# Optimization experiments

Measured on AMD Instinct MI355X. Metric: run time of the kernel, lower is better.

Reference implementation:

```python
import jax, jax.numpy as jnp
import numpy as np

NEG = -1.0e9

def setup_inputs() -> dict:
    key = jax.random.key(0)
    ks = jax.random.split(key, 4)
    B, S, D, DK = 4, 2048, 1024, 128
    inputs = jax.random.normal(ks[0], (B, S, D), dtype=jnp.float32)
    scale = 1.0 / np.sqrt(D)
    Wq = jax.random.normal(ks[1], (D, DK), dtype=jnp.float32) * scale
    Wk = jax.random.normal(ks[2], (D, DK), dtype=jnp.float32) * scale
    Wv = jax.random.normal(ks[3], (D, DK), dtype=jnp.float32) * scale
    bq = jnp.zeros((DK,), dtype=jnp.float32)
    bk = jnp.zeros((DK,), dtype=jnp.float32)
    bv = jnp.zeros((DK,), dtype=jnp.float32)
    return {"inputs": inputs, "Wq": Wq, "bq": bq, "Wk": Wk, "bk": bk, "Wv": Wv, "bv": bv}

def reference(inputs, Wq, bq, Wk, bk, Wv, bv):
    # Q/K/V projections: Dense(d_k) on last dim
    Q = jnp.einsum('bsd,dk->bsk', inputs, Wq) + bq
    K = jnp.einsum('bsd,dk->bsk', inputs, Wk) + bk
    V = jnp.einsum('bsd,dk->bsk', inputs, Wv) + bv
    d_k = Q.shape[-1]
    S = inputs.shape[1]
    # FAITHFUL to original bug: mask = lower-triangular ones, added *-1e9
    # (masks the lower triangle including the diagonal, NOT the upper).
    mask = jnp.tril(jnp.ones((S, S), dtype=inputs.dtype))
    scores = jnp.einsum('bqk,bsk->bqs', Q, K) / jnp.sqrt(jnp.asarray(d_k, inputs.dtype))
    masked_scores = scores + mask * NEG  # [B, S, S]
    attn = jax.nn.softmax(masked_scores, axis=-1)
    out = jnp.einsum('bqs,bsk->bqk', attn, V)  # [B, S, d_k]
    return out
```

## Files before the change

### kernel.cpp

```cpp
#include <hip/hip_runtime.h>
#include <hip/hip_bf16.h>

typedef __attribute__((ext_vector_type(8))) short bf16x8;
typedef __attribute__((ext_vector_type(4))) float f32x4;

#define QSCALE 0.088388347648318447f

__device__ __forceinline__ unsigned short f2bf(float f) {
  __hip_bfloat16 h = __float2bfloat16(f);
  unsigned short u;
  __builtin_memcpy(&u, &h, 2);
  return u;
}
__device__ __forceinline__ float bf2f(unsigned short u) {
  unsigned int x = ((unsigned int)u) << 16;
  float f; __builtin_memcpy(&f, &x, 4);
  return f;
}

__device__ __forceinline__ void gload_lds16(void* lds, const void* g) {
  __builtin_amdgcn_global_load_lds(
      (const __attribute__((address_space(1))) unsigned int*)g,
      (__attribute__((address_space(3))) unsigned int*)lds, 16, 0, 0);
}

__global__ __launch_bounds__(256) void cvt(const float* __restrict__ x,
                                           unsigned short* __restrict__ xb,
                                           const float* __restrict__ Wq,
                                           const float* __restrict__ Wk,
                                           const float* __restrict__ Wv,
                                           unsigned short* __restrict__ Wt) {
  const int bid = blockIdx.x;
  if (bid < 4096) {
    int i = (bid * 256 + threadIdx.x) * 8;
    float4 v0 = *reinterpret_cast<const float4*>(x + i);
    float4 v1 = *reinterpret_cast<const float4*>(x + i + 4);
    ushort4 o0, o1;
    o0.x = f2bf(v0.x); o0.y = f2bf(v0.y); o0.z = f2bf(v0.z); o0.w = f2bf(v0.w);
    o1.x = f2bf(v1.x); o1.y = f2bf(v1.y); o1.z = f2bf(v1.z); o1.w = f2bf(v1.w);
    *reinterpret_cast<ushort4*>(xb + i) = o0;
    *reinterpret_cast<ushort4*>(xb + i + 4) = o1;
  } else {
    int idx = (bid - 4096) * 256 + threadIdx.x;
    int n = idx >> 10, d = idx & 1023;
    const float* W = (n < 128) ? Wq : (n < 256 ? Wk : Wv);
    float v = W[d * 128 + (n & 127)];
    if (n < 128) v *= QSCALE;
    Wt[idx] = f2bf(v);
  }
}

__global__ __launch_bounds__(256) void proj_gemm(
    const unsigned short* __restrict__ Xb, const unsigned short* __restrict__ Wt,
    const float* __restrict__ bq, const float* __restrict__ bk, const float* __restrict__ bv,
    unsigned short* __restrict__ Qb, unsigned short* __restrict__ Kb,
    unsigned short* __restrict__ Vt) {
  __shared__ unsigned short sA[64 * 64];
  __shared__ unsigned short sB[64 * 64];
  const int nt = blockIdx.x % 6;
  const int mt = blockIdx.x / 6;
  const int m0 = mt * 64;
  const int n0 = nt * 64;
  const int tid = threadIdx.x;
  const int lane = tid & 63;
  const int w = tid >> 6;
  const int r = lane & 15, g = lane >> 4;
  const int wm = (w >> 1) * 32, wn = (w & 1) * 32;

  f32x4 acc[2][2];
  #pragma unroll
  for (int mi = 0; mi < 2; ++mi)
    #pragma unroll
    for (int ni = 0; ni < 2; ++ni)
      acc[mi][ni] = (f32x4){0.f, 0.f, 0.f, 0.f};

  const char* Ab = (const char*)Xb;
  const char* Bb = (const char*)Wt;
  char* sAb = (char*)sA;
  char* sBb = (char*)sB;

  for (int k0 = 0; k0 < 1024; k0 += 64) {
    #pragma unroll
    for (int j = 0; j < 2; ++j) {
      int f = j * 4096 + tid * 16;
      int row = f >> 7;
      int colb = f & 127;
      gload_lds16(sAb + f, Ab + ((size_t)(m0 + row) * 1024 + k0) * 2 + colb);
      gload_lds16(sBb + f, Bb + ((size_t)(n0 + row) * 1024 + k0) * 2 + colb);
    }
    __syncthreads();
    #pragma unroll
    for (int kk = 0; kk < 2; ++kk) {
      bf16x8 af[2], bfr[2];
      #pragma unroll
      for (int mi = 0; mi < 2; ++mi)
        af[mi] = *reinterpret_cast<const bf16x8*>(sA + (wm + mi * 16 + r) * 64 + kk * 32 + g * 8);
      #pragma unroll
      for (int ni = 0; ni < 2; ++ni)
        bfr[ni] = *reinterpret_cast<const bf16x8*>(sB + (wn + ni * 16 + r) * 64 + kk * 32 + g * 8);
      #pragma unroll
      for (int mi = 0; mi < 2; ++mi)
        #pragma unroll
        for (int ni = 0; ni < 2; ++ni)
          acc[mi][ni] = __builtin_amdgcn_mfma_f32_16x16x32_bf16(af[mi], bfr[ni], acc[mi][ni], 0, 0, 0);
    }
    __syncthreads();
  }

  const float* bias = (nt < 2) ? bq : (nt < 4 ? bk : bv);
  const float bsc = (nt < 2) ? QSCALE : 1.0f;
  #pragma unroll
  for (int mi = 0; mi < 2; ++mi) {
    #pragma unroll
    for (int ni = 0; ni < 2; ++ni) {
      const int colg = n0 + wn + ni * 16 + r;
      const int colm = colg & 127;
      const float bias_v = bias[colm] * bsc;
      #pragma unroll
      for (int e = 0; e < 4; ++e) {
        const int row = m0 + wm + mi * 16 + g * 4 + e;
        const unsigned short hh = f2bf(acc[mi][ni][e] + bias_v);
        if (nt < 2) Qb[(size_t)row * 128 + colm] = hh;
        else if (nt < 4) Kb[(size_t)row * 128 + colm] = hh;
        else {
          const int bb = row >> 11, s = row & 2047;
          Vt[((size_t)bb * 128 + colm) * 2048 + s] = hh;
        }
      }
    }
  }
}

__global__ __launch_bounds__(512, 4) void attn(
    const unsigned short* __restrict__ Qb, const unsigned short* __restrict__ Kb,
    const unsigned short* __restrict__ Vt,
    float* __restrict__ po, float* __restrict__ pl) {
  __shared__ char sK[2][8192];
  __shared__ char sV[2][8192];
  __shared__ unsigned short pbuf_s[8][512];
  const int tid = threadIdx.x;
  const int lane = tid & 63;
  const int w = tid >> 6;
  const int r = lane & 15, g = lane >> 4;
  const int sig = blockIdx.x & 7;
  const int b = (blockIdx.x >> 3) & 3;
  const int p = blockIdx.x >> 5;

  const char* Kg = (const char*)(Kb + (size_t)b * 2048 * 128);
  const char* Vg = (const char*)(Vt + (size_t)b * 128 * 2048);
  unsigned short* pbuf = pbuf_s[w];

  const int krow = tid >> 4;
  const int kcol = ((tid & 15) * 16) ^ ((krow & 7) * 16);
  const int vrow = tid >> 2;
  const int vcol = ((tid & 3) * 16) ^ ((vrow & 3) * 16);

  for (int phase = 0; phase < 2; ++phase) {
    const int t = phase ? (15 - p) : p;
    const int q0b = t << 7;
    const int ntiles = (2048 - q0b) >> 5;
    const int q0w = q0b + w * 16;

    const unsigned short* Q = Qb + (size_t)(b * 2048 + q0w) * 128;
    bf16x8 qf[4];
    #pragma unroll
    for (int kk = 0; kk < 4; ++kk)
      qf[kk] = *reinterpret_cast<const bf16x8*>(Q + r * 128 + kk * 32 + g * 8);

    f32x4 o[8];
    #pragma unroll
    for (int ni = 0; ni < 8; ++ni) o[ni] = (f32x4){0.f, 0.f, 0.f, 0.f};
    float l[4];
    #pragma unroll
    for (int e = 0; e < 4; ++e) l[e] = 0.f;

    const int nT = (ntiles > sig) ? ((ntiles - sig + 7) >> 3) : 0;

    if (nT > 0) {
      const int s0 = q0b + (sig << 5);
      gload_lds16(&sK[0][tid * 16], Kg + (size_t)(s0 + krow) * 256 + kcol);
      gload_lds16(&sV[0][tid * 16], Vg + (size_t)vrow * 4096 + (size_t)s0 * 2 + vcol);
    }
    for (int it = 0; it < nT; ++it) {
      const int cur = it & 1;
      const int s0 = q0b + ((sig + (it << 3)) << 5);
      if (it + 1 < nT) {
        const int s1 = s0 + 256;
        gload_lds16(&sK[cur ^ 1][tid * 16], Kg + (size_t)(s1 + krow) * 256 + kcol);
        gload_lds16(&sV[cur ^ 1][tid * 16], Vg + (size_t)vrow * 4096 + (size_t)s1 * 2 + vcol);
        asm volatile("s_waitcnt vmcnt(2)" ::: "memory");
      } else {
        asm volatile("s_waitcnt vmcnt(0)" ::: "memory");
      }
      asm volatile("s_barrier" ::: "memory");

      f32x4 st[2];
      #pragma unroll
      for (int sj = 0; sj < 2; ++sj) {
        f32x4 a = (f32x4){0.f, 0.f, 0.f, 0.f};
        #pragma unroll
        for (int kk = 0; kk < 4; ++kk) {
          const bf16x8 kf = *reinterpret_cast<const bf16x8*>(
              &sK[cur][(sj * 16 + r) * 256 + (((kk * 64 + g * 16) ^ ((r & 7) * 16)))]);
          a = __builtin_amdgcn_mfma_f32_16x16x32_bf16(qf[kk], kf, a, 0, 0, 0);
        }
        st[sj] = a;
      }
      #pragma unroll
      for (int sj = 0; sj < 2; ++sj) {
        const int s = s0 + sj * 16 + r;
        #pragma unroll
        for (int e = 0; e < 4; ++e) {
          const int q = q0w + g * 4 + e;
          st[sj][e] = (s <= q) ? 0.f : __expf(st[sj][e]);
        }
      }
      #pragma unroll
      for (int e = 0; e < 4; ++e) l[e] += st[0][e] + st[1][e];

      #pragma unroll
      for (int sj = 0; sj < 2; ++sj)
        #pragma unroll
        for (int e = 0; e < 4; ++e)
          pbuf[(g * 4 + e) * 32 + sj * 16 + r] = f2bf(st[sj][e]);
      asm volatile("s_waitcnt lgkmcnt(0)" ::: "memory");
      __builtin_amdgcn_sched_barrier(0);
      const bf16x8 pa = *reinterpret_cast<const bf16x8*>(&pbuf[r * 32 + g * 8]);

      #pragma unroll
      for (int ni = 0; ni < 8; ++ni) {
        const bf16x8 vf = *reinterpret_cast<const bf16x8*>(
            &sV[cur][(ni * 16 + r) * 64 + ((g * 16) ^ ((r & 3) * 16))]);
        o[ni] = __builtin_amdgcn_mfma_f32_16x16x32_bf16(pa, vf, o[ni], 0, 0, 0);
      }
      asm volatile("s_waitcnt lgkmcnt(0)" ::: "memory");
      __builtin_amdgcn_sched_barrier(0);
      asm volatile("s_barrier" ::: "memory");
    }

    #pragma unroll
    for (int off = 1; off < 16; off <<= 1)
      #pragma unroll
      for (int e = 0; e < 4; ++e)
        l[e] += __shfl_xor(l[e], off, 64);

    const size_t pb = ((size_t)((b * 16 + t) * 8 + sig)) * 16384;
    #pragma unroll
    for (int ni = 0; ni < 8; ++ni)
      #pragma unroll
      for (int e = 0; e < 4; ++e)
        po[pb + (size_t)(w * 16 + g * 4 + e) * 128 + ni * 16 + r] = o[ni][e];
    if (r == 0) {
      #pragma unroll
      for (int e = 0; e < 4; ++e)
        pl[((size_t)((b * 16 + t) * 8 + sig)) * 128 + w * 16 + g * 4 + e] = l[e];
    }
  }
}

__global__ __launch_bounds__(256) void combine(const float* __restrict__ po,
                                               const float* __restrict__ pl,
                                               const unsigned short* __restrict__ Vt,
                                               float* __restrict__ out) {
  const int bid = blockIdx.x;
  if (bid < 4096) {
    const int idx = bid * 256 + threadIdx.x;
    const int d = idx & 127;
    const int gq = idx >> 7;
    const int b = gq >> 11, q = gq & 2047;
    if (q == 2047) return;
    const int qt = q >> 7, row = q & 127;
    const size_t base = (size_t)(b * 16 + qt) * 8;
    float o = 0.f, l = 0.f;
    #pragma unroll
    for (int s = 0; s < 8; ++s) {
      o += po[(base + s) * 16384 + row * 128 + d];
      l += pl[(base + s) * 128 + row];
    }
    out[idx] = (l > 0.f) ? o / l : 0.f;
  } else {
    const int seg = bid - 4096;
    const int b = seg >> 5;
    const int w = threadIdx.x >> 6;
    const int lane = threadIdx.x & 63;
    const int dk = (seg & 31) * 4 + w;
    const unsigned short* row = Vt + (size_t)(b * 128 + dk) * 2048;
    float s = 0.f;
    for (int i = lane; i < 2048; i += 64) s += bf2f(row[i]);
    #pragma unroll
    for (int off = 32; off > 0; off >>= 1) s += __shfl_down(s, off, 64);
    if (lane == 0) out[(size_t)(b * 2048 + 2047) * 128 + dk] = s * (1.0f / 2048.0f);
  }
}

extern "C" void kernel_launch(void* const* d_in, const int* in_sizes, int n_in,
                              void* d_out, int out_size, void* d_ws, size_t ws_size,
                              hipStream_t stream) {
  const float* x  = (const float*)d_in[0];
  const float* Wq = (const float*)d_in[1];
  const float* bq = (const float*)d_in[2];
  const float* Wk = (const float*)d_in[3];
  const float* bk = (const float*)d_in[4];
  const float* Wv = (const float*)d_in[5];
  const float* bv = (const float*)d_in[6];
  float* out = (float*)d_out;
  char* ws = (char*)d_ws;
  unsigned short* Xb = (unsigned short*)(ws);
  unsigned short* Wt = (unsigned short*)(ws + (size_t)(16u << 20));
  unsigned short* Qb = (unsigned short*)(ws + (size_t)(17u << 20));
  unsigned short* Kb = (unsigned short*)(ws + (size_t)(19u << 20));
  unsigned short* Vt = (unsigned short*)(ws + (size_t)(21u << 20));
  float* po = (float*)(ws + (size_t)(24u << 20));
  float* pl = (float*)(ws + (size_t)(56u << 20));

  hipLaunchKernelGGL(cvt, dim3(5632), dim3(256), 0, stream, x, Xb, Wq, Wk, Wv, Wt);
  hipLaunchKernelGGL(proj_gemm, dim3(768), dim3(256), 0, stream,
                     Xb, Wt, bq, bk, bv, Qb, Kb, Vt);
  hipLaunchKernelGGL(attn, dim3(256), dim3(512), 0, stream, Qb, Kb, Vt, po, pl);
  hipLaunchKernelGGL(combine, dim3(4224), dim3(256), 0, stream, po, pl, Vt, out);
}
```

Measured before the change: 68.39 us.

## Double-buffer LDS tiles in projection GEMM to overlap loads with MFMA

```diff
diff --git a/kernel.cpp b/kernel.cpp
--- a/kernel.cpp
+++ b/kernel.cpp
@@ -55,8 +55,8 @@
     const float* __restrict__ bq, const float* __restrict__ bk, const float* __restrict__ bv,
     unsigned short* __restrict__ Qb, unsigned short* __restrict__ Kb,
     unsigned short* __restrict__ Vt) {
-  __shared__ unsigned short sA[64 * 64];
-  __shared__ unsigned short sB[64 * 64];
+  __shared__ char sA[2][8192];
+  __shared__ char sB[2][8192];
   const int nt = blockIdx.x % 6;
   const int mt = blockIdx.x / 6;
   const int m0 = mt * 64;
@@ -76,35 +76,51 @@
 
   const char* Ab = (const char*)Xb;
   const char* Bb = (const char*)Wt;
-  char* sAb = (char*)sA;
-  char* sBb = (char*)sB;
-
-  for (int k0 = 0; k0 < 1024; k0 += 64) {
-    #pragma unroll
-    for (int j = 0; j < 2; ++j) {
-      int f = j * 4096 + tid * 16;
-      int row = f >> 7;
-      int colb = f & 127;
-      gload_lds16(sAb + f, Ab + ((size_t)(m0 + row) * 1024 + k0) * 2 + colb);
-      gload_lds16(sBb + f, Bb + ((size_t)(n0 + row) * 1024 + k0) * 2 + colb);
-    }
-    __syncthreads();
+  const int f0 = tid * 16;
+  const int f1 = 4096 + tid * 16;
+  const int ra0 = f0 >> 7, ca0 = f0 & 127;
+  const int ra1 = f1 >> 7, ca1 = f1 & 127;
+
+  {
+    gload_lds16(&sA[0][f0], Ab + ((size_t)(m0 + ra0) * 1024 + 0) * 2 + ca0);
+    gload_lds16(&sB[0][f0], Bb + ((size_t)(n0 + ra0) * 1024 + 0) * 2 + ca0);
+    gload_lds16(&sA[0][f1], Ab + ((size_t)(m0 + ra1) * 1024 + 0) * 2 + ca1);
+    gload_lds16(&sB[0][f1], Bb + ((size_t)(n0 + ra1) * 1024 + 0) * 2 + ca1);
+  }
+  for (int it = 0; it < 16; ++it) {
+    const int cur = it & 1;
+    if (it + 1 < 16) {
+      const int k1 = (it + 1) * 64;
+      gload_lds16(&sA[cur ^ 1][f0], Ab + ((size_t)(m0 + ra0) * 1024 + k1) * 2 + ca0);
+      gload_lds16(&sB[cur ^ 1][f0], Bb + ((size_t)(n0 + ra0) * 1024 + k1) * 2 + ca0);
+      gload_lds16(&sA[cur ^ 1][f1], Ab + ((size_t)(m0 + ra1) * 1024 + k1) * 2 + ca1);
+      gload_lds16(&sB[cur ^ 1][f1], Bb + ((size_t)(n0 + ra1) * 1024 + k1) * 2 + ca1);
+      asm volatile("s_waitcnt vmcnt(4)" ::: "memory");
+    } else {
+      asm volatile("s_waitcnt vmcnt(0)" ::: "memory");
+    }
+    asm volatile("s_barrier" ::: "memory");
+
+    const unsigned short* cA = (const unsigned short*)sA[cur];
+    const unsigned short* cB = (const unsigned short*)sB[cur];
     #pragma unroll
     for (int kk = 0; kk < 2; ++kk) {
       bf16x8 af[2], bfr[2];
       #pragma unroll
       for (int mi = 0; mi < 2; ++mi)
-        af[mi] = *reinterpret_cast<const bf16x8*>(sA + (wm + mi * 16 + r) * 64 + kk * 32 + g * 8);
+        af[mi] = *reinterpret_cast<const bf16x8*>(cA + (wm + mi * 16 + r) * 64 + kk * 32 + g * 8);
       #pragma unroll
       for (int ni = 0; ni < 2; ++ni)
-        bfr[ni] = *reinterpret_cast<const bf16x8*>(sB + (wn + ni * 16 + r) * 64 + kk * 32 + g * 8);
+        bfr[ni] = *reinterpret_cast<const bf16x8*>(cB + (wn + ni * 16 + r) * 64 + kk * 32 + g * 8);
       #pragma unroll
       for (int mi = 0; mi < 2; ++mi)
         #pragma unroll
         for (int ni = 0; ni < 2; ++ni)
           acc[mi][ni] = __builtin_amdgcn_mfma_f32_16x16x32_bf16(af[mi], bfr[ni], acc[mi][ni], 0, 0, 0);
     }
-    __syncthreads();
+    asm volatile("s_waitcnt lgkmcnt(0)" ::: "memory");
+    __builtin_amdgcn_sched_barrier(0);
+    asm volatile("s_barrier" ::: "memory");
   }
 
   const float* bias = (nt < 2) ? bq : (nt < 4 ? bk : bv);
```

Result: slower. 69.94 us (+2.3%).
